# Kernel tuning notes

Hardware: AMD Instinct MI355X
Metric: run time of the kernel (lower is better)

## Reference

```python
import jax, jax.numpy as jnp
import numpy as np

D_MODEL = 1024
NUM_HEADS = 16
D_K = D_MODEL // NUM_HEADS


def setup_inputs() -> dict:
    key = jax.random.key(0)
    ks = jax.random.split(key, 11)
    B, T = 4, 2048
    s = 1.0 / np.sqrt(D_MODEL)
    inp = {
        "query": jax.random.normal(ks[0], (B, T, D_MODEL), jnp.float32),
        "key": jax.random.normal(ks[1], (B, T, D_MODEL), jnp.float32),
        "value": jax.random.normal(ks[2], (B, T, D_MODEL), jnp.float32),
        "Wq": jax.random.uniform(ks[3], (D_MODEL, D_MODEL), jnp.float32, -s, s),
        "bq": jax.random.uniform(ks[4], (D_MODEL,), jnp.float32, -s, s),
        "Wk": jax.random.uniform(ks[5], (D_MODEL, D_MODEL), jnp.float32, -s, s),
        "bk": jax.random.uniform(ks[6], (D_MODEL,), jnp.float32, -s, s),
        "Wv": jax.random.uniform(ks[7], (D_MODEL, D_MODEL), jnp.float32, -s, s),
        "bv": jax.random.uniform(ks[8], (D_MODEL,), jnp.float32, -s, s),
        "Wo": jax.random.uniform(ks[9], (D_MODEL, D_MODEL), jnp.float32, -s, s),
        "bo": jax.random.uniform(ks[10], (D_MODEL,), jnp.float32, -s, s),
    }
    return inp


def _split_heads(x):
    B, T, _ = x.shape
    return x.reshape(B, T, NUM_HEADS, D_K).transpose(0, 2, 1, 3)  # (B,H,T,dk)


def reference(query, key, value, Wq, bq, Wk, bk, Wv, bv, Wo, bo):
    q = _split_heads(query @ Wq + bq)   # (B,H,Tq,dk)
    k = _split_heads(key @ Wk + bk)     # (B,H,Tk,dk)
    v = _split_heads(value @ Wv + bv)   # (B,H,Tk,dk)
    scale = 1.0 / jnp.sqrt(jnp.asarray(D_K, q.dtype))
    scores = jnp.einsum("bhqd,bhkd->bhqk", q, k) * scale
    weights = jax.nn.softmax(scores, axis=-1)
    attn = jnp.einsum("bhqk,bhkd->bhqd", weights, v)  # (B,H,Tq,dk)
    B, H, T, dk = attn.shape
    attn = attn.transpose(0, 2, 1, 3).reshape(B, T, H * dk)
    return attn @ Wo + bo
```

## Files before the change

### kernel.cpp

```cpp
#include <hip/hip_runtime.h>
#include <hip/hip_bf16.h>
#include <stdint.h>


typedef __bf16 bf16x8 __attribute__((ext_vector_type(8)));
typedef short  v4s    __attribute__((ext_vector_type(4)));
typedef float  f32x4  __attribute__((ext_vector_type(4)));

#define LOG2E 1.44269504088896340736f

static __device__ __forceinline__ uint32_t f2bf(float x) {
  uint32_t u = __float_as_uint(x);
  u += 0x7fffu + ((u >> 16) & 1u);
  return u >> 16;
}
#if __has_builtin(__builtin_amdgcn_cvt_pk_bf16_f32)
static __device__ __forceinline__ uint32_t pk2bf(float a, float b) {
  typedef __bf16 b2 __attribute__((ext_vector_type(2)));
  union { b2 v; uint32_t u; } x;
  x.v = __builtin_amdgcn_cvt_pk_bf16_f32(a, b);
  return x.u;
}
#else
static __device__ __forceinline__ uint32_t pk2bf(float a, float b) {
  return f2bf(a) | (f2bf(b) << 16);
}
#endif
static __device__ __forceinline__ void gl2lds16(const void* g, void* l) {
  __builtin_amdgcn_global_load_lds(
      (const __attribute__((address_space(1))) uint32_t*)g,
      (__attribute__((address_space(3))) uint32_t*)l, 16, 0, 0);
}

__global__ void convert_inputs(const float* __restrict__ q, const float* __restrict__ k,
                               const float* __restrict__ v, uint16_t* __restrict__ qo,
                               uint16_t* __restrict__ ko, uint16_t* __restrict__ vo) {
  const float* src = blockIdx.y == 0 ? q : (blockIdx.y == 1 ? k : v);
  uint16_t*    dst = blockIdx.y == 0 ? qo : (blockIdx.y == 1 ? ko : vo);
  size_t idx = ((size_t)blockIdx.x * 256 + threadIdx.x) * 8;
  float4 a = *(const float4*)(src + idx);
  float4 b = *(const float4*)(src + idx + 4);
  uint4 o;
  o.x = pk2bf(a.x, a.y); o.y = pk2bf(a.z, a.w);
  o.z = pk2bf(b.x, b.y); o.w = pk2bf(b.z, b.w);
  *(uint4*)(dst + idx) = o;
}

__global__ void transpose_weights(const float* __restrict__ Wq, const float* __restrict__ Wk,
                                  const float* __restrict__ Wv, const float* __restrict__ Wo,
                                  uint16_t* __restrict__ out) {
  __shared__ float t[32][33];
  const float* W = blockIdx.z == 0 ? Wq : blockIdx.z == 1 ? Wk : blockIdx.z == 2 ? Wv : Wo;
  uint16_t* O = out + (size_t)blockIdx.z * 1048576;
  int tx = threadIdx.x & 31, ty = threadIdx.x >> 5;
  int r0 = blockIdx.y * 32, c0 = blockIdx.x * 32;
#pragma unroll
  for (int i = 0; i < 4; i++) t[ty + i * 8][tx] = W[(size_t)(r0 + ty + i * 8) * 1024 + c0 + tx];
  __syncthreads();
#pragma unroll
  for (int i = 0; i < 4; i++)
    O[(size_t)(c0 + ty + i * 8) * 1024 + r0 + tx] = (uint16_t)f2bf(t[tx][ty + i * 8]);
}

static __device__ __forceinline__ void gemm_body(
    const uint16_t* __restrict__ A, const uint16_t* __restrict__ Bt,
    const float* __restrict__ bias, void* __restrict__ Cout,
    int N, int K, int mode, float oscale, int mBase, int nBase,
    uint16_t* __restrict__ lA, uint16_t* __restrict__ lB) {
  int tid = threadIdx.x, wave = tid >> 6, lane = tid & 63;
  int q = lane >> 4, c = lane & 15;
  int wrow = wave & 1, wcol = wave >> 1;
  f32x4 acc[4][4] = {};

  int swz = ((lane & 7) ^ (lane >> 3)) * 8;
  const uint16_t* gA = A + (size_t)(mBase + wave * 32 + (lane >> 3)) * K + swz;
  const uint16_t* gB = Bt + (size_t)(nBase + wave * 32 + (lane >> 3)) * K + swz;
  int cs = c & 7;

  for (int kt = 0; kt < K / 64; kt++) {
    __syncthreads();
    int k0 = kt * 64;
#pragma unroll
    for (int it = 0; it < 4; it++) {
      gl2lds16(gA + (size_t)(it * 8) * K + k0, &lA[(wave * 32 + it * 8) * 64]);
      gl2lds16(gB + (size_t)(it * 8) * K + k0, &lB[(wave * 32 + it * 8) * 64]);
    }
    __syncthreads();
#pragma unroll
    for (int kk = 0; kk < 2; kk++) {
      bf16x8 af[4], bfr[4];
#pragma unroll
      for (int i = 0; i < 4; i++)
        af[i] = *(const bf16x8*)&lA[(wrow * 64 + i * 16 + c) * 64 + ((kk * 4 + q) ^ cs) * 8];
#pragma unroll
      for (int j = 0; j < 4; j++)
        bfr[j] = *(const bf16x8*)&lB[(wcol * 64 + j * 16 + c) * 64 + ((kk * 4 + q) ^ cs) * 8];
#pragma unroll
      for (int i = 0; i < 4; i++)
#pragma unroll
        for (int j = 0; j < 4; j++)
          acc[i][j] = __builtin_amdgcn_mfma_f32_16x16x32_bf16(af[i], bfr[j], acc[i][j], 0, 0, 0);
    }
  }

  float bb[4];
#pragma unroll
  for (int j = 0; j < 4; j++) bb[j] = bias[nBase + wcol * 64 + j * 16 + c];

  if (mode == 0) {
    float* Co = (float*)Cout;
#pragma unroll
    for (int i = 0; i < 4; i++)
#pragma unroll
      for (int j = 0; j < 4; j++) {
        int row = mBase + wrow * 64 + i * 16 + q * 4;
        int col = nBase + wcol * 64 + j * 16 + c;
#pragma unroll
        for (int r = 0; r < 4; r++) Co[(size_t)(row + r) * N + col] = acc[i][j][r] + bb[j];
      }
  } else if (mode == 1) {
    uint16_t* Co = (uint16_t*)Cout;
#pragma unroll
    for (int i = 0; i < 4; i++)
#pragma unroll
      for (int j = 0; j < 4; j++) {
        int row = mBase + wrow * 64 + i * 16 + q * 4;
        int col = nBase + wcol * 64 + j * 16 + c;
#pragma unroll
        for (int r = 0; r < 4; r++)
          Co[(size_t)(row + r) * N + col] = (uint16_t)f2bf((acc[i][j][r] + bb[j]) * oscale);
      }
  } else {
    uint16_t* Co = (uint16_t*)Cout;
#pragma unroll
    for (int i = 0; i < 4; i++)
#pragma unroll
      for (int j = 0; j < 4; j++) {
        int n = nBase + wcol * 64 + j * 16 + c;
        int h = n >> 6, d = n & 63;
        int m = mBase + wrow * 64 + i * 16 + q * 4;
        int b = m >> 11, t = m & 2047;
        uint32_t lo = pk2bf(acc[i][j][0] + bb[j], acc[i][j][1] + bb[j]);
        uint32_t hi = pk2bf(acc[i][j][2] + bb[j], acc[i][j][3] + bb[j]);
        *(uint2*)(Co + (size_t)((b * 16 + h) * 64 + d) * 2048 + t) = make_uint2(lo, hi);
      }
  }
}

__global__ __launch_bounds__(256, 2)
void gemm_qkv(const uint16_t* __restrict__ qb, const uint16_t* __restrict__ kb,
              const uint16_t* __restrict__ vb, const uint16_t* __restrict__ Wtq,
              const uint16_t* __restrict__ Wtk, const uint16_t* __restrict__ Wtv,
              const float* __restrict__ bq, const float* __restrict__ bk,
              const float* __restrict__ bv, uint16_t* __restrict__ Qp,
              uint16_t* __restrict__ Kp, uint16_t* __restrict__ Vt, float cs) {
  __shared__ uint16_t lA[8192], lB[8192];
  int id = blockIdx.x + (blockIdx.y << 3) + (blockIdx.z << 9);
  int xcd = id & 7, j = id >> 3;
  int by = xcd * 8 + (j & 7);
  int bx = (j >> 3) & 7;
  int z  = j >> 6;
  const uint16_t* A  = z == 0 ? qb : (z == 1 ? kb : vb);
  const uint16_t* Bt = z == 0 ? Wtq : (z == 1 ? Wtk : Wtv);
  const float* bias  = z == 0 ? bq : (z == 1 ? bk : bv);
  void* C            = z == 0 ? (void*)Qp : (z == 1 ? (void*)Kp : (void*)Vt);
  int mode   = z == 2 ? 2 : 1;
  float os   = z == 0 ? cs : 1.0f;
  gemm_body(A, Bt, bias, C, 1024, 1024, mode, os, by * 128, bx * 128, lA, lB);
}

__global__ __launch_bounds__(256, 2)
void gemm_out(const uint16_t* __restrict__ A, const uint16_t* __restrict__ Bt,
              const float* __restrict__ bias, float* __restrict__ C) {
  __shared__ uint16_t lA[8192], lB[8192];
  int id = blockIdx.x + (blockIdx.y << 3);
  int xcd = id & 7, j = id >> 3;
  int by = xcd * 8 + (j & 7);
  int bx = j >> 3;
  gemm_body(A, Bt, bias, C, 1024, 1024, 0, 1.0f, by * 128, bx * 128, lA, lB);
}

__global__ __launch_bounds__(256, 2)
void attn(const uint16_t* __restrict__ Qp, const uint16_t* __restrict__ Kp,
          const uint16_t* __restrict__ Vt, uint16_t* __restrict__ Ob) {
  __shared__ uint16_t lds[16384];
  int tid = threadIdx.x, wave = tid >> 6, lane = tid & 63;
  int q = lane >> 4, c = lane & 15;
  int cs = c & 7;

  int id = blockIdx.y * 16 + blockIdx.x;
  int wk = (id & 7) * 128 + (id >> 3);
  int qt = wk & 15, bh = wk >> 4;
  int b = bh >> 4, h = bh & 15;
  int qbase = qt * 128;
  int swz = ((lane & 7) ^ (lane >> 3)) * 8;

  {
    const uint16_t* gQ =
        Qp + (size_t)(b * 2048 + qbase + wave * 32 + (lane >> 3)) * 1024 + h * 64 + swz;
#pragma unroll
    for (int it = 0; it < 4; it++)
      gl2lds16(gQ + (size_t)(it * 8) * 1024, &lds[(wave * 32 + it * 8) * 64]);
  }
  __syncthreads();
  bf16x8 qf[2][2];
#pragma unroll
  for (int it = 0; it < 2; it++)
#pragma unroll
    for (int kk = 0; kk < 2; kk++)
      qf[it][kk] =
          *(const bf16x8*)&lds[(wave * 32 + it * 16 + c) * 64 + ((kk * 4 + q) ^ cs) * 8];
  __syncthreads();

  f32x4 o[4][2] = {};
  f32x4 lacc[2] = {};
  const v4s vone = {(short)0x3F80, (short)0x3F80, (short)0x3F80, (short)0x3F80};

  const uint16_t* gK0 =
      Kp + (size_t)(b * 2048 + wave * 16 + (lane >> 3)) * 1024 + h * 64 + swz;
  const uint16_t* gV0 = Vt + (size_t)(bh * 64 + wave * 16 + (lane >> 3)) * 2048 + swz;

#pragma unroll
  for (int it = 0; it < 2; it++) {
    gl2lds16(gK0 + (size_t)(it * 8) * 1024, &lds[(wave * 16 + it * 8) * 64]);
    gl2lds16(gV0 + (size_t)(it * 8) * 2048, &lds[8192 + (wave * 16 + it * 8) * 64]);
  }

  for (int kt = 0; kt < 32; kt++) {
    int cur = kt & 1;
    __syncthreads();

    if (kt < 31) {
      int nb = (cur ^ 1) * 4096;
#pragma unroll
      for (int it = 0; it < 2; it++) {
        gl2lds16(gK0 + (size_t)((kt + 1) * 64 + it * 8) * 1024,
                 &lds[nb + (wave * 16 + it * 8) * 64]);
        gl2lds16(gV0 + (size_t)(it * 8) * 2048 + (kt + 1) * 64,
                 &lds[8192 + nb + (wave * 16 + it * 8) * 64]);
      }
    }

    const uint16_t* sKc = &lds[cur * 4096];
    const uint16_t* sVc = &lds[8192 + cur * 4096];

    f32x4 s0, s1, n0, n1;
    {
      bf16x8 a0 = *(const bf16x8*)&sKc[(c)*64 + (q ^ cs) * 8];
      bf16x8 a1 = *(const bf16x8*)&sKc[(c)*64 + ((4 + q) ^ cs) * 8];
      s0 = __builtin_amdgcn_mfma_f32_16x16x32_bf16(a0, qf[0][0],
                                                   (f32x4){0.f, 0.f, 0.f, 0.f}, 0, 0, 0);
      s0 = __builtin_amdgcn_mfma_f32_16x16x32_bf16(a1, qf[0][1], s0, 0, 0, 0);
      s1 = __builtin_amdgcn_mfma_f32_16x16x32_bf16(a0, qf[1][0],
                                                   (f32x4){0.f, 0.f, 0.f, 0.f}, 0, 0, 0);
      s1 = __builtin_amdgcn_mfma_f32_16x16x32_bf16(a1, qf[1][1], s1, 0, 0, 0);
    }
#pragma unroll
    for (int jt = 0; jt < 4; jt++) {
      if (jt < 3) {
        bf16x8 a0 = *(const bf16x8*)&sKc[((jt + 1) * 16 + c) * 64 + (q ^ cs) * 8];
        bf16x8 a1 = *(const bf16x8*)&sKc[((jt + 1) * 16 + c) * 64 + ((4 + q) ^ cs) * 8];
        n0 = __builtin_amdgcn_mfma_f32_16x16x32_bf16(a0, qf[0][0],
                                                     (f32x4){0.f, 0.f, 0.f, 0.f}, 0, 0, 0);
        n0 = __builtin_amdgcn_mfma_f32_16x16x32_bf16(a1, qf[0][1], n0, 0, 0, 0);
        n1 = __builtin_amdgcn_mfma_f32_16x16x32_bf16(a0, qf[1][0],
                                                     (f32x4){0.f, 0.f, 0.f, 0.f}, 0, 0, 0);
        n1 = __builtin_amdgcn_mfma_f32_16x16x32_bf16(a1, qf[1][1], n1, 0, 0, 0);
      }

      float p00 = __builtin_amdgcn_exp2f(s0[0]), p01 = __builtin_amdgcn_exp2f(s0[1]);
      float p02 = __builtin_amdgcn_exp2f(s0[2]), p03 = __builtin_amdgcn_exp2f(s0[3]);
      float p10 = __builtin_amdgcn_exp2f(s1[0]), p11 = __builtin_amdgcn_exp2f(s1[1]);
      float p12 = __builtin_amdgcn_exp2f(s1[2]), p13 = __builtin_amdgcn_exp2f(s1[3]);
      union { uint32_t u[2]; v4s s4; } pb0, pb1;
      pb0.u[0] = pk2bf(p00, p01); pb0.u[1] = pk2bf(p02, p03);
      pb1.u[0] = pk2bf(p10, p11); pb1.u[1] = pk2bf(p12, p13);

      lacc[0] = __builtin_amdgcn_mfma_f32_16x16x16bf16_1k(vone, pb0.s4, lacc[0], 0, 0, 0);
      lacc[1] = __builtin_amdgcn_mfma_f32_16x16x16bf16_1k(vone, pb1.s4, lacc[1], 0, 0, 0);

#pragma unroll
      for (int mt = 0; mt < 4; mt++) {
        v4s a = *(const v4s*)&sVc[(mt * 16 + c) * 64 + (((jt * 2 + (q >> 1)) ^ cs) * 8) +
                                  (q & 1) * 4];
        o[mt][0] = __builtin_amdgcn_mfma_f32_16x16x16bf16_1k(a, pb0.s4, o[mt][0], 0, 0, 0);
        o[mt][1] = __builtin_amdgcn_mfma_f32_16x16x16bf16_1k(a, pb1.s4, o[mt][1], 0, 0, 0);
      }
      if (jt < 3) { s0 = n0; s1 = n1; }
    }
  }

  float l[2] = {lacc[0][0], lacc[1][0]};

#pragma unroll
  for (int it = 0; it < 2; it++) {
    float inv = 1.0f / l[it];
    size_t trow = (size_t)(b * 2048 + qbase + wave * 32 + it * 16 + c) * 1024 + h * 64;
#pragma unroll
    for (int mt = 0; mt < 4; mt++) {
      uint32_t lo = pk2bf(o[mt][it][0] * inv, o[mt][it][1] * inv);
      uint32_t hi = pk2bf(o[mt][it][2] * inv, o[mt][it][3] * inv);
      *(uint2*)(Ob + trow + mt * 16 + q * 4) = make_uint2(lo, hi);
    }
  }
}

extern "C" void kernel_launch(void* const* d_in, const int* in_sizes, int n_in,
                              void* d_out, int out_size, void* d_ws, size_t ws_size,
                              hipStream_t stream) {
  (void)in_sizes; (void)n_in; (void)out_size; (void)ws_size;
  const float* query = (const float*)d_in[0];
  const float* key_  = (const float*)d_in[1];
  const float* value = (const float*)d_in[2];
  const float* Wq = (const float*)d_in[3]; const float* bq = (const float*)d_in[4];
  const float* Wk = (const float*)d_in[5]; const float* bk = (const float*)d_in[6];
  const float* Wv = (const float*)d_in[7]; const float* bv = (const float*)d_in[8];
  const float* Wo = (const float*)d_in[9]; const float* bo = (const float*)d_in[10];

  const size_t SZ = (size_t)8192 * 1024;
  uint16_t* buf0 = (uint16_t*)d_ws;
  uint16_t* buf1 = buf0 + SZ;
  uint16_t* buf2 = buf1 + SZ;
  uint16_t* buf3 = buf2 + SZ;
  uint16_t* wts  = buf3 + SZ;
  uint16_t* Wtq = wts;
  uint16_t* Wtk = wts + 1048576;
  uint16_t* Wtv = wts + 2097152;
  uint16_t* Wto = wts + 3145728;
  uint16_t* Kp  = wts + 4194304;
  uint16_t* Vt  = Kp + SZ;

  const float Cs = 0.125f * LOG2E;

  convert_inputs<<<dim3(4096, 3), 256, 0, stream>>>(query, key_, value, buf0, buf1, buf2);
  transpose_weights<<<dim3(32, 32, 4), 256, 0, stream>>>(Wq, Wk, Wv, Wo, wts);
  gemm_qkv<<<dim3(8, 64, 3), 256, 0, stream>>>(buf0, buf1, buf2, Wtq, Wtk, Wtv,
                                               bq, bk, bv, buf3, Kp, Vt, Cs);
  attn<<<dim3(16, 64), 256, 0, stream>>>(buf3, Kp, Vt, buf2);
  gemm_out<<<dim3(8, 64), 256, 0, stream>>>(buf2, Wto, bo, (float*)d_out);
}
```

Before: 348.2 us.

## Use K=32 MFMA for PV and row-sum by reordering K rows in LDS

Reorders the K tile in shared memory so that two 16-key score blocks interleave into the operand layout of the 16x16x32 MFMA. This lets P·V and the row-sum accumulation use the 16x16x32 instruction instead of pairs of 16x16x16 calls. The main loop is also unrolled by two over the double buffer, so buffer offsets become compile-time constants. The aim is fewer MFMA issues and wider LDS reads, at the cost of more live score registers and a trickier swizzle that could be wrong or cause bank conflicts.

```diff
diff --git a/kernel.cpp b/kernel.cpp
--- a/kernel.cpp
+++ b/kernel.cpp
@@ -187,6 +187,8 @@
   int tid = threadIdx.x, wave = tid >> 6, lane = tid & 63;
   int q = lane >> 4, c = lane & 15;
   int cs = c & 7;
+  int gq   = (c & 3) | (((c >> 2) & 1) << 2);
+  int rowA = ((c >> 2) << 3) + (c & 3);
 
   int id = blockIdx.y * 16 + blockIdx.x;
   int wk = (id & 7) * 128 + (id >> 3);
@@ -214,80 +216,80 @@
 
   f32x4 o[4][2] = {};
   f32x4 lacc[2] = {};
-  const v4s vone = {(short)0x3F80, (short)0x3F80, (short)0x3F80, (short)0x3F80};
-
-  const uint16_t* gK0 =
-      Kp + (size_t)(b * 2048 + wave * 16 + (lane >> 3)) * 1024 + h * 64 + swz;
+  union { uint32_t u[4]; bf16x8 v; } one8;
+  one8.u[0] = one8.u[1] = one8.u[2] = one8.u[3] = 0x3F803F80u;
+
+  int kchunk = (lane & 7) ^ ((lane >> 3) & 3);
+  const uint16_t* gKa =
+      Kp + (size_t)(b * 2048 + wave * 16 + (lane >> 3)) * 1024 + h * 64 + kchunk * 8;
+  const uint16_t* gKb =
+      Kp + (size_t)(b * 2048 + wave * 16 + 8 + (lane >> 3)) * 1024 + h * 64 + (kchunk ^ 4) * 8;
   const uint16_t* gV0 = Vt + (size_t)(bh * 64 + wave * 16 + (lane >> 3)) * 2048 + swz;
 
-#pragma unroll
-  for (int it = 0; it < 2; it++) {
-    gl2lds16(gK0 + (size_t)(it * 8) * 1024, &lds[(wave * 16 + it * 8) * 64]);
-    gl2lds16(gV0 + (size_t)(it * 8) * 2048, &lds[8192 + (wave * 16 + it * 8) * 64]);
-  }
-
-  for (int kt = 0; kt < 32; kt++) {
-    int cur = kt & 1;
+  auto stage = [&](int tile, int nb) {
+    gl2lds16(gKa + (size_t)(tile * 64) * 1024, &lds[nb + (wave * 16) * 64]);
+    gl2lds16(gKb + (size_t)(tile * 64) * 1024, &lds[nb + (wave * 16 + 8) * 64]);
+    gl2lds16(gV0 + (size_t)(tile * 64), &lds[8192 + nb + (wave * 16) * 64]);
+    gl2lds16(gV0 + (size_t)(8 * 2048) + tile * 64, &lds[8192 + nb + (wave * 16 + 8) * 64]);
+  };
+
+  auto compute = [&](const uint16_t* sKc, const uint16_t* sVc) {
+    f32x4 s[2][2][2];
+#pragma unroll
+    for (int p = 0; p < 2; p++) {
+      const uint16_t* kr = &sKc[(p * 32 + rowA) * 64];
+      bf16x8 aA0 = *(const bf16x8*)&kr[(q ^ gq) * 8];
+      bf16x8 aA1 = *(const bf16x8*)&kr[((4 + q) ^ gq) * 8];
+      bf16x8 aB0 = *(const bf16x8*)&kr[256 + (q ^ gq) * 8];
+      bf16x8 aB1 = *(const bf16x8*)&kr[256 + ((4 + q) ^ gq) * 8];
+      s[p][0][0] = __builtin_amdgcn_mfma_f32_16x16x32_bf16(aA0, qf[0][0],
+                                                           (f32x4){0.f, 0.f, 0.f, 0.f}, 0, 0, 0);
+      s[p][0][0] = __builtin_amdgcn_mfma_f32_16x16x32_bf16(aA1, qf[0][1], s[p][0][0], 0, 0, 0);
+      s[p][0][1] = __builtin_amdgcn_mfma_f32_16x16x32_bf16(aA0, qf[1][0],
+                                                           (f32x4){0.f, 0.f, 0.f, 0.f}, 0, 0, 0);
+      s[p][0][1] = __builtin_amdgcn_mfma_f32_16x16x32_bf16(aA1, qf[1][1], s[p][0][1], 0, 0, 0);
+      s[p][1][0] = __builtin_amdgcn_mfma_f32_16x16x32_bf16(aB0, qf[0][0],
+                                                           (f32x4){0.f, 0.f, 0.f, 0.f}, 0, 0, 0);
+      s[p][1][0] = __builtin_amdgcn_mfma_f32_16x16x32_bf16(aB1, qf[0][1], s[p][1][0], 0, 0, 0);
+      s[p][1][1] = __builtin_amdgcn_mfma_f32_16x16x32_bf16(aB0, qf[1][0],
+                                                           (f32x4){0.f, 0.f, 0.f, 0.f}, 0, 0, 0);
+      s[p][1][1] = __builtin_amdgcn_mfma_f32_16x16x32_bf16(aB1, qf[1][1], s[p][1][1], 0, 0, 0);
+    }
+#pragma unroll
+    for (int p = 0; p < 2; p++) {
+      union { uint32_t u[4]; bf16x8 v; } pb[2];
+#pragma unroll
+      for (int it = 0; it < 2; it++) {
+        float a0 = __builtin_amdgcn_exp2f(s[p][0][it][0]);
+        float a1 = __builtin_amdgcn_exp2f(s[p][0][it][1]);
+        float a2 = __builtin_amdgcn_exp2f(s[p][0][it][2]);
+        float a3 = __builtin_amdgcn_exp2f(s[p][0][it][3]);
+        float b0 = __builtin_amdgcn_exp2f(s[p][1][it][0]);
+        float b1 = __builtin_amdgcn_exp2f(s[p][1][it][1]);
+        float b2 = __builtin_amdgcn_exp2f(s[p][1][it][2]);
+        float b3 = __builtin_amdgcn_exp2f(s[p][1][it][3]);
+        pb[it].u[0] = pk2bf(a0, a1); pb[it].u[1] = pk2bf(a2, a3);
+        pb[it].u[2] = pk2bf(b0, b1); pb[it].u[3] = pk2bf(b2, b3);
+      }
+      lacc[0] = __builtin_amdgcn_mfma_f32_16x16x32_bf16(one8.v, pb[0].v, lacc[0], 0, 0, 0);
+      lacc[1] = __builtin_amdgcn_mfma_f32_16x16x32_bf16(one8.v, pb[1].v, lacc[1], 0, 0, 0);
+#pragma unroll
+      for (int mt = 0; mt < 4; mt++) {
+        bf16x8 vv = *(const bf16x8*)&sVc[(mt * 16 + c) * 64 + (((p * 4 + q) ^ cs) * 8)];
+        o[mt][0] = __builtin_amdgcn_mfma_f32_16x16x32_bf16(vv, pb[0].v, o[mt][0], 0, 0, 0);
+        o[mt][1] = __builtin_amdgcn_mfma_f32_16x16x32_bf16(vv, pb[1].v, o[mt][1], 0, 0, 0);
+      }
+    }
+  };
+
+  stage(0, 0);
+  for (int kt2 = 0; kt2 < 16; kt2++) {
     __syncthreads();
-
-    if (kt < 31) {
-      int nb = (cur ^ 1) * 4096;
-#pragma unroll
-      for (int it = 0; it < 2; it++) {
-        gl2lds16(gK0 + (size_t)((kt + 1) * 64 + it * 8) * 1024,
-                 &lds[nb + (wave * 16 + it * 8) * 64]);
-        gl2lds16(gV0 + (size_t)(it * 8) * 2048 + (kt + 1) * 64,
-                 &lds[8192 + nb + (wave * 16 + it * 8) * 64]);
-      }
-    }
-
-    const uint16_t* sKc = &lds[cur * 4096];
-    const uint16_t* sVc = &lds[8192 + cur * 4096];
-
-    f32x4 s0, s1, n0, n1;
-    {
-      bf16x8 a0 = *(const bf16x8*)&sKc[(c)*64 + (q ^ cs) * 8];
-      bf16x8 a1 = *(const bf16x8*)&sKc[(c)*64 + ((4 + q) ^ cs) * 8];
-      s0 = __builtin_amdgcn_mfma_f32_16x16x32_bf16(a0, qf[0][0],
-                                                   (f32x4){0.f, 0.f, 0.f, 0.f}, 0, 0, 0);
-      s0 = __builtin_amdgcn_mfma_f32_16x16x32_bf16(a1, qf[0][1], s0, 0, 0, 0);
-      s1 = __builtin_amdgcn_mfma_f32_16x16x32_bf16(a0, qf[1][0],
-                                                   (f32x4){0.f, 0.f, 0.f, 0.f}, 0, 0, 0);
-      s1 = __builtin_amdgcn_mfma_f32_16x16x32_bf16(a1, qf[1][1], s1, 0, 0, 0);
-    }
-#pragma unroll
-    for (int jt = 0; jt < 4; jt++) {
-      if (jt < 3) {
-        bf16x8 a0 = *(const bf16x8*)&sKc[((jt + 1) * 16 + c) * 64 + (q ^ cs) * 8];
-        bf16x8 a1 = *(const bf16x8*)&sKc[((jt + 1) * 16 + c) * 64 + ((4 + q) ^ cs) * 8];
-        n0 = __builtin_amdgcn_mfma_f32_16x16x32_bf16(a0, qf[0][0],
-                                                     (f32x4){0.f, 0.f, 0.f, 0.f}, 0, 0, 0);
-        n0 = __builtin_amdgcn_mfma_f32_16x16x32_bf16(a1, qf[0][1], n0, 0, 0, 0);
-        n1 = __builtin_amdgcn_mfma_f32_16x16x32_bf16(a0, qf[1][0],
-                                                     (f32x4){0.f, 0.f, 0.f, 0.f}, 0, 0, 0);
-        n1 = __builtin_amdgcn_mfma_f32_16x16x32_bf16(a1, qf[1][1], n1, 0, 0, 0);
-      }
-
-      float p00 = __builtin_amdgcn_exp2f(s0[0]), p01 = __builtin_amdgcn_exp2f(s0[1]);
-      float p02 = __builtin_amdgcn_exp2f(s0[2]), p03 = __builtin_amdgcn_exp2f(s0[3]);
-      float p10 = __builtin_amdgcn_exp2f(s1[0]), p11 = __builtin_amdgcn_exp2f(s1[1]);
-      float p12 = __builtin_amdgcn_exp2f(s1[2]), p13 = __builtin_amdgcn_exp2f(s1[3]);
-      union { uint32_t u[2]; v4s s4; } pb0, pb1;
-      pb0.u[0] = pk2bf(p00, p01); pb0.u[1] = pk2bf(p02, p03);
-      pb1.u[0] = pk2bf(p10, p11); pb1.u[1] = pk2bf(p12, p13);
-
-      lacc[0] = __builtin_amdgcn_mfma_f32_16x16x16bf16_1k(vone, pb0.s4, lacc[0], 0, 0, 0);
-      lacc[1] = __builtin_amdgcn_mfma_f32_16x16x16bf16_1k(vone, pb1.s4, lacc[1], 0, 0, 0);
-
-#pragma unroll
-      for (int mt = 0; mt < 4; mt++) {
-        v4s a = *(const v4s*)&sVc[(mt * 16 + c) * 64 + (((jt * 2 + (q >> 1)) ^ cs) * 8) +
-                                  (q & 1) * 4];
-        o[mt][0] = __builtin_amdgcn_mfma_f32_16x16x16bf16_1k(a, pb0.s4, o[mt][0], 0, 0, 0);
-        o[mt][1] = __builtin_amdgcn_mfma_f32_16x16x16bf16_1k(a, pb1.s4, o[mt][1], 0, 0, 0);
-      }
-      if (jt < 3) { s0 = n0; s1 = n1; }
-    }
+    stage(kt2 * 2 + 1, 4096);
+    compute(&lds[0], &lds[8192]);
+    __syncthreads();
+    if (kt2 < 15) stage(kt2 * 2 + 2, 0);
+    compute(&lds[4096], &lds[12288]);
   }
 
   float l[2] = {lacc[0][0], lacc[1][0]};
```

Measured after the change: 329.9 us. 5.3% less time.
